# Kernel optimization log

Hardware: AMD Instinct MI355X
Metric: run time of the kernel (lower is better)

## Reference

```python
import jax, jax.numpy as jnp
import numpy as np

N_QUBITS = 14
LATENT = 14
DEPTH = 4
BATCH = 256
DIM = 1 << N_QUBITS  # 16384 amplitudes

# PennyLane convention: wire 0 is the most-significant bit of the flat state index.
_idx = np.arange(DIM)
_bits = (_idx[None, :] >> (N_QUBITS - 1 - np.arange(N_QUBITS)[:, None])) & 1  # [n_qubits, DIM]
_parity = np.sum(_bits[:-1] * _bits[1:], axis=0) % 2  # adjacent-pair CZ chain parity
CZ_SIGNS = jnp.asarray(1.0 - 2.0 * _parity, dtype=jnp.complex64)  # [DIM]
Z_SIGNS = jnp.asarray(1 - 2 * _bits[:LATENT], dtype=jnp.float32)  # [LATENT, DIM]


def _rx(t):
    c = jnp.cos(0.5 * t) + 0j
    s = -1j * jnp.sin(0.5 * t)
    m = jnp.stack([jnp.stack([c, s], -1), jnp.stack([s, c], -1)], -2)
    return m.astype(jnp.complex64)


def _ry(t):
    c = jnp.cos(0.5 * t)
    s = jnp.sin(0.5 * t)
    m = jnp.stack([jnp.stack([c, -s], -1), jnp.stack([s, c], -1)], -2)
    return m.astype(jnp.complex64)


def _rz(t):
    e = jnp.exp(-0.5j * t.astype(jnp.complex64))
    z = jnp.zeros_like(e)
    m = jnp.stack([jnp.stack([e, z], -1), jnp.stack([z, jnp.conj(e)], -1)], -2)
    return m.astype(jnp.complex64)


def _apply_1q(state, mat, wire):
    # state: [B, DIM]; mat: [2,2] (shared) or [B,2,2] (per-sample)
    B = state.shape[0]
    left = 1 << wire
    right = 1 << (N_QUBITS - wire - 1)
    st = state.reshape(B, left, 2, right)
    if mat.ndim == 3:
        st = jnp.einsum('bij,bajc->baic', mat, st)
    else:
        st = jnp.einsum('ij,bajc->baic', mat, st)
    return st.reshape(B, DIM)


def setup_inputs() -> dict:
    key = jax.random.key(0)
    k1, k2, k3, k4 = jax.random.split(key, 4)
    conditioning = jax.random.normal(k1, (BATCH, LATENT), dtype=jnp.float32)
    lim = 1.0 / np.sqrt(LATENT)
    W_enc = jax.random.uniform(k2, (N_QUBITS, LATENT), jnp.float32, -lim, lim)
    b_enc = jax.random.uniform(k3, (N_QUBITS,), jnp.float32, -lim, lim)
    # TorchLayer default init: U(0, 2*pi)
    weights = jax.random.uniform(k4, (DEPTH, N_QUBITS, 3), jnp.float32, 0.0, 2.0 * np.pi)
    return {"conditioning": conditioning, "W_enc": W_enc, "b_enc": b_enc, "weights": weights}


def reference(conditioning, W_enc, b_enc, weights):
    # encode: Linear + SiLU -> per-wire rotation angles [B, n_qubits]
    emb = conditioning @ W_enc.T + b_enc
    emb = emb * jax.nn.sigmoid(emb)
    B = emb.shape[0]

    state = jnp.zeros((B, DIM), jnp.complex64).at[:, 0].set(1.0)

    # angle encoding: RX(v) then RY(v) on each wire (per-sample gates)
    for w in range(N_QUBITS):
        v = emb[:, w]
        U = jnp.einsum('bij,bjk->bik', _ry(v), _rx(v))  # [B,2,2]
        state = _apply_1q(state, U, w)

    # variational layers: RZ, RX, RY per wire (shared gates), then CZ chain
    for d in range(DEPTH):
        for w in range(N_QUBITS):
            p = weights[d, w]
            U = _ry(p[2]) @ _rx(p[1]) @ _rz(p[0])  # [2,2]
            state = _apply_1q(state, U, w)
        state = state * CZ_SIGNS  # all adjacent CZs fused into one diagonal

    probs = state.real ** 2 + state.imag ** 2  # [B, DIM]
    latent = probs @ Z_SIGNS.T  # <Z_w> for w in range(LATENT) -> [B, LATENT]

    # F.layer_norm over last dim, no affine params
    mu = jnp.mean(latent, axis=-1, keepdims=True)
    var = jnp.var(latent, axis=-1, keepdims=True)
    return (latent - mu) / jnp.sqrt(var + 1e-5)
```

## Files before the change

kernel.cpp:

```cpp
#include <hip/hip_runtime.h>
#include <math.h>

#define NQ    14
#define DIM   16384
#define DEPTH 4

typedef __attribute__((ext_vector_type(2))) float f2;
typedef __attribute__((ext_vector_type(4))) float f4;

__device__ __forceinline__ f2 cmul(f2 a, f2 b) {
    return (f2){a.x*b.x - a.y*b.y, a.x*b.y + a.y*b.x};
}
__device__ __forceinline__ f2 cmac2(f2 x, f2 u, f2 us, f2 y, f2 v, f2 vs) {
    f2 r = x.xx * u;
    r += x.yy * us;
    r += y.xx * v;
    r += y.yy * vs;
    return r;
}

__device__ __forceinline__ int sw(int e) { return e ^ ((e >> 6) & 0xF); }

__device__ __forceinline__ float czsgn(int e) {
    return (__popc(e & (e >> 1)) & 1) ? -1.0f : 1.0f;
}

template<int PASS>
__device__ __forceinline__ int emap3(int t, int s, int l) {
    if (PASS == 0) return (l << 11) | (s << 10) | t;
    if (PASS == 1) return (s << 13) | ((t >> 8) << 11) | (l << 8) | (t & 255);
    if (PASS == 2) return (s << 13) | ((t >> 5) << 8) | (l << 5) | (t & 31);
    if (PASS == 3) return (s << 13) | ((t >> 7) << 10) | (((t >> 2) & 15) << 6)
                        | (((t >> 6) & 1) << 5) | (l << 2) | (t & 3);
    return (s << 12) | (t << 2) | l;
}

template<int PASS>
__device__ __forceinline__ void do_pass(f2* st, const f4 (*gl)[4], int t,
                                        bool mulsign)
{
    constexpr int NS    = (PASS == 4) ? 4 : 2;
    constexpr int NL    = (PASS == 4) ? 4 : 8;
    constexpr int NG    = (PASS == 4) ? 2 : 3;
    constexpr int QBASE = (PASS == 4) ? 12 : 3 * PASS;

    #pragma unroll 1
    for (int s = 0; s < NS; ++s) {
        f2 a[NL];
        #pragma unroll
        for (int l = 0; l < NL; ++l)
            a[l] = st[sw(emap3<PASS>(t, s, l))];
        if (mulsign) {
            #pragma unroll
            for (int l = 0; l < NL; ++l)
                a[l] *= czsgn(emap3<PASS>(t, s, l));
        }
        #pragma unroll
        for (int g = 0; g < NG; ++g) {
            const int mask = (PASS == 4) ? (2 >> g) : (4 >> g);
            f4 g0 = gl[QBASE + g][0];
            f4 g1 = gl[QBASE + g][1];
            f4 g2 = gl[QBASE + g][2];
            f4 g3 = gl[QBASE + g][3];
            #pragma unroll
            for (int l = 0; l < NL; ++l) {
                if (l & mask) continue;
                const int j = l | mask;
                f2 x = a[l], y = a[j];
                a[l] = cmac2(x, g0.xy, g0.zw, y, g1.xy, g1.zw);
                a[j] = cmac2(x, g2.xy, g2.zw, y, g3.xy, g3.zw);
            }
        }
        #pragma unroll
        for (int l = 0; l < NL; ++l)
            st[sw(emap3<PASS>(t, s, l))] = a[l];
    }
}

__device__ __forceinline__ void do_pass4_final(f2* st, const f4 (*gl)[4], int t,
                                               float& SU, float& A0, float& A1,
                                               float& B0, float& B1)
{
    SU = A0 = A1 = B0 = B1 = 0.f;
    #pragma unroll 1
    for (int s = 0; s < 4; ++s) {
        f2 a[4];
        #pragma unroll
        for (int l = 0; l < 4; ++l)
            a[l] = st[sw(emap3<4>(t, s, l))];
        #pragma unroll
        for (int g = 0; g < 2; ++g) {
            const int mask = 2 >> g;
            f4 g0 = gl[12 + g][0];
            f4 g1 = gl[12 + g][1];
            f4 g2 = gl[12 + g][2];
            f4 g3 = gl[12 + g][3];
            #pragma unroll
            for (int l = 0; l < 4; ++l) {
                if (l & mask) continue;
                const int j = l | mask;
                f2 x = a[l], y = a[j];
                a[l] = cmac2(x, g0.xy, g0.zw, y, g1.xy, g1.zw);
                a[j] = cmac2(x, g2.xy, g2.zw, y, g3.xy, g3.zw);
            }
        }
        float p0 = a[0].x*a[0].x + a[0].y*a[0].y;
        float p1 = a[1].x*a[1].x + a[1].y*a[1].y;
        float p2 = a[2].x*a[2].x + a[2].y*a[2].y;
        float p3 = a[3].x*a[3].x + a[3].y*a[3].y;
        float G  = (p0 + p1) + (p2 + p3);
        SU += G;
        A0 += (s & 2) ? -G : G;
        A1 += (s & 1) ? -G : G;
        B0 += (p0 + p1) - (p2 + p3);
        B1 += (p0 - p1) + (p2 - p3);
    }
}

__device__ __forceinline__ void do_layer(f2* st, const f4 (*gl)[4], int t,
                                         bool mulsign)
{
    do_pass<0>(st, gl, t, mulsign); __syncthreads();
    do_pass<1>(st, gl, t, false);   __syncthreads();
    do_pass<2>(st, gl, t, false);   __syncthreads();
    do_pass<3>(st, gl, t, false);   __syncthreads();
    do_pass<4>(st, gl, t, false);   __syncthreads();
}

__global__ __launch_bounds__(1024)
void qlg_kernel(const float* __restrict__ cond,
                const float* __restrict__ Wenc,
                const float* __restrict__ benc,
                const float* __restrict__ wts,
                float* __restrict__ out)
{
    __shared__ f2 st[DIM];
    __shared__ f4 gates[DEPTH][NQ][4];
    __shared__ f2 qv[NQ][2];
    __shared__ f2 Phi[128];
    __shared__ f2 Plo[128];
    __shared__ float embS[NQ];
    __shared__ float wred[16][NQ];
    __shared__ float lat[NQ];

    const int b = blockIdx.x;
    const int t = threadIdx.x;

    if (t < NQ) {
        float s = benc[t];
        #pragma unroll
        for (int k = 0; k < NQ; ++k) s += cond[b*NQ + k] * Wenc[t*NQ + k];
        embS[t] = s / (1.0f + __expf(-s));
    }
    if (t >= 64 && t < 64 + DEPTH*NQ) {
        const int gi = t - 64;
        const int d = gi / NQ, w = gi % NQ;
        const float p0 = wts[(d*NQ + w)*3 + 0];
        const float p1 = wts[(d*NQ + w)*3 + 1];
        const float p2 = wts[(d*NQ + w)*3 + 2];
        float s0, c0, s1, c1, s2, c2;
        sincosf(0.5f*p0, &s0, &c0);
        sincosf(0.5f*p1, &s1, &c1);
        sincosf(0.5f*p2, &s2, &c2);
        f2 e0  = (f2){c0, -s0};
        f2 e0c = (f2){c0,  s0};
        f2 is1 = (f2){0.f, -s1};
        f2 m00 = c1 * e0;
        f2 m01 = cmul(is1, e0c);
        f2 m10 = cmul(is1, e0);
        f2 m11 = c1 * e0c;
        f2 u00 = c2*m00 - s2*m10;
        f2 u01 = c2*m01 - s2*m11;
        f2 u10 = s2*m00 + c2*m10;
        f2 u11 = s2*m01 + c2*m11;
        gates[d][w][0] = (f4){u00.x, u00.y, -u00.y, u00.x};
        gates[d][w][1] = (f4){u01.x, u01.y, -u01.y, u01.x};
        gates[d][w][2] = (f4){u10.x, u10.y, -u10.y, u10.x};
        gates[d][w][3] = (f4){u11.x, u11.y, -u11.y, u11.x};
    }
    __syncthreads();

    if (t < NQ) {
        float v = embS[t];
        float s, c;
        sincosf(0.5f*v, &s, &c);
        f2 a0 = (f2){c*c,  s*s};
        f2 a1 = (f2){s*c, -s*c};
        f2 u00 = gates[0][t][0].xy, u01 = gates[0][t][1].xy;
        f2 u10 = gates[0][t][2].xy, u11 = gates[0][t][3].xy;
        qv[t][0] = cmul(u00, a0) + cmul(u01, a1);
        qv[t][1] = cmul(u10, a0) + cmul(u11, a1);
    }
    __syncthreads();

    if (t < 128) {
        f2 p = qv[0][(t >> 6) & 1];
        #pragma unroll
        for (int w = 1; w <= 6; ++w) p = cmul(p, qv[w][(t >> (6 - w)) & 1]);
        Phi[t] = p;
    } else if (t < 256) {
        const int j = t - 128;
        f2 p = qv[7][(j >> 6) & 1];
        #pragma unroll
        for (int w = 8; w <= 13; ++w) p = cmul(p, qv[w][(j >> (13 - w)) & 1]);
        Plo[j] = p;
    }
    __syncthreads();

    #pragma unroll
    for (int l = 0; l < 16; ++l) {
        const int e = (l << 10) | t;
        f2 v = cmul(Phi[e >> 7], Plo[e & 127]);
        st[sw(e)] = v * czsgn(e);
    }
    __syncthreads();

    do_layer(st, gates[1], t, false);
    do_layer(st, gates[2], t, true);
    {
        const f4 (*gl)[4] = gates[3];
        do_pass<0>(st, gl, t, true);  __syncthreads();
        do_pass<1>(st, gl, t, false); __syncthreads();
        do_pass<2>(st, gl, t, false); __syncthreads();
        do_pass<3>(st, gl, t, false); __syncthreads();
        float SU, A0, A1, B0, B1;
        do_pass4_final(st, gl, t, SU, A0, A1, B0, B1);

        const int lane = t & 63, wv = t >> 6;
        #pragma unroll
        for (int w = 0; w < NQ; ++w) {
            float v;
            if      (w == 0)  v = A0;
            else if (w == 1)  v = A1;
            else if (w == 12) v = B0;
            else if (w == 13) v = B1;
            else              v = ((t >> (11 - w)) & 1) ? -SU : SU;
            #pragma unroll
            for (int off = 32; off > 0; off >>= 1) v += __shfl_down(v, off, 64);
            if (lane == 0) wred[wv][w] = v;
        }
    }
    __syncthreads();
    if (t < NQ) {
        float s = 0.f;
        #pragma unroll
        for (int k = 0; k < 16; ++k) s += wred[k][t];
        lat[t] = s;
    }
    __syncthreads();
    if (t < NQ) {
        float mu = 0.f;
        #pragma unroll
        for (int k = 0; k < NQ; ++k) mu += lat[k];
        mu *= (1.0f / NQ);
        float var = 0.f;
        #pragma unroll
        for (int k = 0; k < NQ; ++k) { float dv = lat[k] - mu; var += dv*dv; }
        var *= (1.0f / NQ);
        out[b*NQ + t] = (lat[t] - mu) * rsqrtf(var + 1e-5f);
    }
}

extern "C" void kernel_launch(void* const* d_in, const int* in_sizes, int n_in,
                              void* d_out, int out_size, void* d_ws, size_t ws_size,
                              hipStream_t stream)
{
    (void)n_in; (void)d_ws; (void)ws_size; (void)out_size;
    const float* cond = (const float*)d_in[0];
    const float* Wenc = (const float*)d_in[1];
    const float* benc = (const float*)d_in[2];
    const float* wts  = (const float*)d_in[3];
    float* out = (float*)d_out;
    const int B = in_sizes[0] / NQ;
    qlg_kernel<<<dim3(B), dim3(1024), 0, stream>>>(cond, Wenc, benc, wts, out);
}
```

Before: 103.3 us.

## Apply 7 qubits per LDS sweep using register and cross-lane DPP exchanges

Each variational layer is restructured from five LDS passes of 2-3 qubits into two sweeps of 7 qubits. Three qubits are applied in registers and four through cross-lane exchanges (DPP row shuffles and ds_swizzle). This cuts the LDS read/write round trips and barriers per layer from five to two, at the cost of more cross-lane instructions and redone index mapping. The final sweep's expectation-value bookkeeping is remapped to match the new qubit placement.

```diff
diff --git a/kernel.cpp b/kernel.cpp
--- a/kernel.cpp
+++ b/kernel.cpp
@@ -25,106 +25,119 @@
     return (__popc(e & (e >> 1)) & 1) ? -1.0f : 1.0f;
 }
 
-template<int PASS>
-__device__ __forceinline__ int emap3(int t, int s, int l) {
-    if (PASS == 0) return (l << 11) | (s << 10) | t;
-    if (PASS == 1) return (s << 13) | ((t >> 8) << 11) | (l << 8) | (t & 255);
-    if (PASS == 2) return (s << 13) | ((t >> 5) << 8) | (l << 5) | (t & 31);
-    if (PASS == 3) return (s << 13) | ((t >> 7) << 10) | (((t >> 2) & 15) << 6)
-                        | (((t >> 6) & 1) << 5) | (l << 2) | (t & 3);
-    return (s << 12) | (t << 2) | l;
-}
-
-template<int PASS>
-__device__ __forceinline__ void do_pass(f2* st, const f4 (*gl)[4], int t,
-                                        bool mulsign)
-{
-    constexpr int NS    = (PASS == 4) ? 4 : 2;
-    constexpr int NL    = (PASS == 4) ? 4 : 8;
-    constexpr int NG    = (PASS == 4) ? 2 : 3;
-    constexpr int QBASE = (PASS == 4) ? 12 : 3 * PASS;
-
+template<int CTRL>
+__device__ __forceinline__ f2 dpp2(f2 v) {
+    union U { f2 f; int i[2]; } u, r;
+    u.f = v;
+    r.i[0] = __builtin_amdgcn_update_dpp(0, u.i[0], CTRL, 0xF, 0xF, true);
+    r.i[1] = __builtin_amdgcn_update_dpp(0, u.i[1], CTRL, 0xF, 0xF, true);
+    return r.f;
+}
+__device__ __forceinline__ f2 swzx4(f2 v) {
+    union U { f2 f; int i[2]; } u, r;
+    u.f = v;
+    r.i[0] = __builtin_amdgcn_ds_swizzle(u.i[0], 0x101F);
+    r.i[1] = __builtin_amdgcn_ds_swizzle(u.i[1], 0x101F);
+    return r.f;
+}
+template<int XB> __device__ __forceinline__ f2 lxchg(f2 v);
+template<> __device__ __forceinline__ f2 lxchg<1>(f2 v) { return dpp2<0xB1>(v); }
+template<> __device__ __forceinline__ f2 lxchg<2>(f2 v) { return dpp2<0x4E>(v); }
+template<> __device__ __forceinline__ f2 lxchg<4>(f2 v) { return swzx4(v); }
+template<> __device__ __forceinline__ f2 lxchg<8>(f2 v) { return dpp2<0x128>(v); }
+
+template<int SWEEP>
+__device__ __forceinline__ int emapS(int t, int s, int l) {
+    if (SWEEP == 0)
+        return (l << 11) | ((t & 15) << 7)
+             | (((t >> 6) & 1) << 6) | (((t >> 7) & 1) << 5) | (((t >> 8) & 1) << 4)
+             | (((t >> 5) & 1) << 3) | (((t >> 9) & 1) << 2) | (s << 1) | ((t >> 4) & 1);
+    return (s << 13) | (((t >> 4) & 63) << 7) | (l << 4) | (t & 15);
+}
+
+template<int MASK>
+__device__ __forceinline__ void reg_gate(f2 a[8], const f4* G) {
+    f4 g0 = G[0], g1 = G[1], g2 = G[2], g3 = G[3];
+    #pragma unroll
+    for (int l = 0; l < 8; ++l) {
+        if (l & MASK) continue;
+        const int j = l | MASK;
+        f2 x = a[l], y = a[j];
+        a[l] = cmac2(x, g0.xy, g0.zw, y, g1.xy, g1.zw);
+        a[j] = cmac2(x, g2.xy, g2.zw, y, g3.xy, g3.zw);
+    }
+}
+
+template<int XB>
+__device__ __forceinline__ void lane_gate(f2 a[8], const f4* G, int t) {
+    const bool hi = (t & XB) != 0;
+    f4 c1 = G[hi ? 3 : 0];
+    f4 c2 = G[hi ? 2 : 1];
+    #pragma unroll
+    for (int l = 0; l < 8; ++l) {
+        f2 p = lxchg<XB>(a[l]);
+        a[l] = cmac2(a[l], c1.xy, c1.zw, p, c2.xy, c2.zw);
+    }
+}
+
+template<int SWEEP>
+__device__ __forceinline__ void do_sweep(f2* st, const f4 (*gl)[4], int t,
+                                         bool mulsign)
+{
+    constexpr int QB = (SWEEP == 0) ? 0 : 7;
     #pragma unroll 1
-    for (int s = 0; s < NS; ++s) {
-        f2 a[NL];
-        #pragma unroll
-        for (int l = 0; l < NL; ++l)
-            a[l] = st[sw(emap3<PASS>(t, s, l))];
+    for (int s = 0; s < 2; ++s) {
+        f2 a[8];
+        #pragma unroll
+        for (int l = 0; l < 8; ++l) a[l] = st[sw(emapS<SWEEP>(t, s, l))];
         if (mulsign) {
             #pragma unroll
-            for (int l = 0; l < NL; ++l)
-                a[l] *= czsgn(emap3<PASS>(t, s, l));
+            for (int l = 0; l < 8; ++l) a[l] *= czsgn(emapS<SWEEP>(t, s, l));
         }
-        #pragma unroll
-        for (int g = 0; g < NG; ++g) {
-            const int mask = (PASS == 4) ? (2 >> g) : (4 >> g);
-            f4 g0 = gl[QBASE + g][0];
-            f4 g1 = gl[QBASE + g][1];
-            f4 g2 = gl[QBASE + g][2];
-            f4 g3 = gl[QBASE + g][3];
-            #pragma unroll
-            for (int l = 0; l < NL; ++l) {
-                if (l & mask) continue;
-                const int j = l | mask;
-                f2 x = a[l], y = a[j];
-                a[l] = cmac2(x, g0.xy, g0.zw, y, g1.xy, g1.zw);
-                a[j] = cmac2(x, g2.xy, g2.zw, y, g3.xy, g3.zw);
-            }
-        }
-        #pragma unroll
-        for (int l = 0; l < NL; ++l)
-            st[sw(emap3<PASS>(t, s, l))] = a[l];
-    }
-}
-
-__device__ __forceinline__ void do_pass4_final(f2* st, const f4 (*gl)[4], int t,
-                                               float& SU, float& A0, float& A1,
-                                               float& B0, float& B1)
-{
-    SU = A0 = A1 = B0 = B1 = 0.f;
+        reg_gate<4>(a, gl[QB + 0]);
+        reg_gate<2>(a, gl[QB + 1]);
+        reg_gate<1>(a, gl[QB + 2]);
+        lane_gate<8>(a, gl[QB + 3], t);
+        lane_gate<4>(a, gl[QB + 4], t);
+        lane_gate<2>(a, gl[QB + 5], t);
+        lane_gate<1>(a, gl[QB + 6], t);
+        #pragma unroll
+        for (int l = 0; l < 8; ++l) st[sw(emapS<SWEEP>(t, s, l))] = a[l];
+    }
+}
+
+__device__ __forceinline__ void do_sweep_final(f2* st, const f4 (*gl)[4], int t,
+        float& SU, float& A0, float& Q7, float& Q8, float& Q9)
+{
+    SU = A0 = Q7 = Q8 = Q9 = 0.f;
     #pragma unroll 1
-    for (int s = 0; s < 4; ++s) {
-        f2 a[4];
-        #pragma unroll
-        for (int l = 0; l < 4; ++l)
-            a[l] = st[sw(emap3<4>(t, s, l))];
-        #pragma unroll
-        for (int g = 0; g < 2; ++g) {
-            const int mask = 2 >> g;
-            f4 g0 = gl[12 + g][0];
-            f4 g1 = gl[12 + g][1];
-            f4 g2 = gl[12 + g][2];
-            f4 g3 = gl[12 + g][3];
-            #pragma unroll
-            for (int l = 0; l < 4; ++l) {
-                if (l & mask) continue;
-                const int j = l | mask;
-                f2 x = a[l], y = a[j];
-                a[l] = cmac2(x, g0.xy, g0.zw, y, g1.xy, g1.zw);
-                a[j] = cmac2(x, g2.xy, g2.zw, y, g3.xy, g3.zw);
-            }
-        }
+    for (int s = 0; s < 2; ++s) {
+        f2 a[8];
+        #pragma unroll
+        for (int l = 0; l < 8; ++l) a[l] = st[sw(emapS<1>(t, s, l))];
+        reg_gate<4>(a, gl[7]);
+        reg_gate<2>(a, gl[8]);
+        reg_gate<1>(a, gl[9]);
+        lane_gate<8>(a, gl[10], t);
+        lane_gate<4>(a, gl[11], t);
+        lane_gate<2>(a, gl[12], t);
+        lane_gate<1>(a, gl[13], t);
         float p0 = a[0].x*a[0].x + a[0].y*a[0].y;
         float p1 = a[1].x*a[1].x + a[1].y*a[1].y;
         float p2 = a[2].x*a[2].x + a[2].y*a[2].y;
         float p3 = a[3].x*a[3].x + a[3].y*a[3].y;
-        float G  = (p0 + p1) + (p2 + p3);
+        float p4 = a[4].x*a[4].x + a[4].y*a[4].y;
+        float p5 = a[5].x*a[5].x + a[5].y*a[5].y;
+        float p6 = a[6].x*a[6].x + a[6].y*a[6].y;
+        float p7 = a[7].x*a[7].x + a[7].y*a[7].y;
+        float e0 = p0 + p1, e1 = p2 + p3, e2 = p4 + p5, e3 = p6 + p7;
+        float G = (e0 + e1) + (e2 + e3);
         SU += G;
-        A0 += (s & 2) ? -G : G;
-        A1 += (s & 1) ? -G : G;
-        B0 += (p0 + p1) - (p2 + p3);
-        B1 += (p0 - p1) + (p2 - p3);
-    }
-}
-
-__device__ __forceinline__ void do_layer(f2* st, const f4 (*gl)[4], int t,
-                                         bool mulsign)
-{
-    do_pass<0>(st, gl, t, mulsign); __syncthreads();
-    do_pass<1>(st, gl, t, false);   __syncthreads();
-    do_pass<2>(st, gl, t, false);   __syncthreads();
-    do_pass<3>(st, gl, t, false);   __syncthreads();
-    do_pass<4>(st, gl, t, false);   __syncthreads();
+        A0 += s ? -G : G;
+        Q7 += (e0 + e1) - (e2 + e3);
+        Q8 += (e0 - e1) + (e2 - e3);
+        Q9 += (p0 - p1) + (p2 - p3) + (p4 - p5) + (p6 - p7);
+    }
 }
 
 __global__ __launch_bounds__(1024)
@@ -215,26 +228,25 @@
     }
     __syncthreads();
 
-    do_layer(st, gates[1], t, false);
-    do_layer(st, gates[2], t, true);
+    do_sweep<0>(st, gates[1], t, false); __syncthreads();
+    do_sweep<1>(st, gates[1], t, false); __syncthreads();
+    do_sweep<0>(st, gates[2], t, true);  __syncthreads();
+    do_sweep<1>(st, gates[2], t, false); __syncthreads();
+    do_sweep<0>(st, gates[3], t, true);  __syncthreads();
+    float SU, A0, Q7, Q8, Q9;
+    do_sweep_final(st, gates[3], t, SU, A0, Q7, Q8, Q9);
+
     {
-        const f4 (*gl)[4] = gates[3];
-        do_pass<0>(st, gl, t, true);  __syncthreads();
-        do_pass<1>(st, gl, t, false); __syncthreads();
-        do_pass<2>(st, gl, t, false); __syncthreads();
-        do_pass<3>(st, gl, t, false); __syncthreads();
-        float SU, A0, A1, B0, B1;
-        do_pass4_final(st, gl, t, SU, A0, A1, B0, B1);
-
         const int lane = t & 63, wv = t >> 6;
         #pragma unroll
         for (int w = 0; w < NQ; ++w) {
             float v;
-            if      (w == 0)  v = A0;
-            else if (w == 1)  v = A1;
-            else if (w == 12) v = B0;
-            else if (w == 13) v = B1;
-            else              v = ((t >> (11 - w)) & 1) ? -SU : SU;
+            if      (w == 0) v = A0;
+            else if (w == 7) v = Q7;
+            else if (w == 8) v = Q8;
+            else if (w == 9) v = Q9;
+            else if (w <= 6) v = ((t >> (10 - w)) & 1) ? -SU : SU;
+            else             v = ((t >> (13 - w)) & 1) ? -SU : SU;
             #pragma unroll
             for (int off = 32; off > 0; off >>= 1) v += __shfl_down(v, off, 64);
             if (lane == 0) wred[wv][w] = v;
```

Measured after the change: 103.7 us. Within noise of the previous version (+0.4%).
